# Kernel tuning notes

Hardware: AMD Instinct MI355X
Metric: run time of the kernel (lower is better)

The kernel has to match this reference:

```python
import jax, jax.numpy as jnp
import numpy as np

N, E, H = 50000, 300000, 8  # nodes, edges, FeaStConv heads (PyG default)


def _lin_init(k, fan_in, fan_out):
    k1, k2 = jax.random.split(k)
    s = 1.0 / np.sqrt(fan_in)
    w = jax.random.uniform(k1, (fan_in, fan_out), jnp.float32, -s, s)
    b = jax.random.uniform(k2, (fan_out,), jnp.float32, -s, s)
    return w, b


def _conv_init(k, cin, cout):
    k1, k2 = jax.random.split(k)
    w = jax.random.normal(k1, (cin, H * cout), jnp.float32) * 0.1   # weight
    u = jax.random.normal(k2, (cin, H), jnp.float32) * 0.1          # attention u
    c = jnp.zeros((H,), jnp.float32)                                 # attention bias
    b = jnp.zeros((cout,), jnp.float32)                              # output bias
    return w, u, c, b


def setup_inputs() -> dict:
    key = jax.random.key(0)
    ks = jax.random.split(key, 10)
    x = jax.random.normal(ks[0], (N, 3), jnp.float32)
    src = jax.random.randint(ks[1], (E,), 0, N)
    dst = jax.random.randint(ks[2], (E,), 0, N)
    dst = jnp.where(src == dst, (dst + 1) % N, dst)  # no self loops in raw edge list
    edge_index = jnp.stack([src, dst]).astype(jnp.int64)
    labels = (jax.random.uniform(ks[3], (N, 1)) < 0.1).astype(jnp.float32)
    lin1_w, lin1_b = _lin_init(ks[4], 3, 16)
    c1_w, c1_u, c1_c, c1_b = _conv_init(ks[5], 16, 32)
    c2_w, c2_u, c2_c, c2_b = _conv_init(ks[6], 32, 64)
    c3_w, c3_u, c3_c, c3_b = _conv_init(ks[7], 64, 128)
    lin2_w, lin2_b = _lin_init(ks[8], 128, 1024)
    lin3_w, lin3_b = _lin_init(ks[9], 1024, 1)
    return dict(x=x, edge_index=edge_index, labels=labels,
                lin1_w=lin1_w, lin1_b=lin1_b,
                c1_w=c1_w, c1_u=c1_u, c1_c=c1_c, c1_b=c1_b,
                c2_w=c2_w, c2_u=c2_u, c2_c=c2_c, c2_b=c2_b,
                c3_w=c3_w, c3_u=c3_u, c3_c=c3_c, c3_b=c3_b,
                lin2_w=lin2_w, lin2_b=lin2_b, lin3_w=lin3_w, lin3_b=lin3_b)


def feast_conv(x, src, dst, W, u, c, b):
    """PyG FeaStConv: gather x_i/x_j, head-softmax attention on (x_j - x_i),
    per-edge weighted sum over heads, mean-scatter to destination nodes."""
    n = x.shape[0]
    loop = jnp.arange(n, dtype=src.dtype)
    s = jnp.concatenate([src, loop])  # add self loops (PyG default)
    d = jnp.concatenate([dst, loop])
    xi = x[d]
    xj = x[s]
    q = jax.nn.softmax((xj - xi) @ u + c, axis=-1)           # [E+N, H]
    m = (xj @ W).reshape(xj.shape[0], H, -1)                  # [E+N, H, O]
    msg = jnp.einsum('eh,eho->eo', q, m)                      # [E+N, O]
    agg = jax.ops.segment_sum(msg, d, num_segments=n)
    cnt = jax.ops.segment_sum(jnp.ones_like(d, dtype=msg.dtype), d, num_segments=n)
    return agg / cnt[:, None] + b                             # mean aggregation + bias


def reference(x, edge_index, labels,
              lin1_w, lin1_b,
              c1_w, c1_u, c1_c, c1_b,
              c2_w, c2_u, c2_c, c2_b,
              c3_w, c3_u, c3_c, c3_b,
              lin2_w, lin2_b, lin3_w, lin3_b):
    src, dst = edge_index[0], edge_index[1]
    h = jax.nn.relu(x @ lin1_w + lin1_b)
    h = jax.nn.relu(feast_conv(h, src, dst, c1_w, c1_u, c1_c, c1_b))
    h = jax.nn.relu(feast_conv(h, src, dst, c2_w, c2_u, c2_c, c2_b))
    h = jax.nn.relu(feast_conv(h, src, dst, c3_w, c3_u, c3_c, c3_b))
    h = jax.nn.relu(h @ lin2_w + lin2_b)
    p = jax.nn.sigmoid(h @ lin3_w + lin3_b)                   # [N, 1]
    # generate_weights: class-balanced per-element BCE weights
    n = labels.shape[0]
    pos = jnp.sum(labels)
    neg = n - pos
    w = jnp.where(labels == 1, n / (2.0 * pos), n / (2.0 * neg))
    # torch-style BCE with log clamped at -100
    bce = -(labels * jnp.clip(jnp.log(p), -100.0, None)
            + (1.0 - labels) * jnp.clip(jnp.log(1.0 - p), -100.0, None))
    loss = jnp.mean(w * bce)
    return loss, p
```

## Files before the change

kernel.cpp:

```cpp
#include <hip/hip_runtime.h>
#include <math.h>

#define NN 50000
#define NE 300000

typedef short s8v __attribute__((ext_vector_type(8)));
typedef float f4v __attribute__((ext_vector_type(4)));

__device__ inline unsigned short f2bf(float f) {
    union { float f; unsigned int u; } v; v.f = f;
    unsigned int r = v.u + 0x7FFFu + ((v.u >> 16) & 1u);
    return (unsigned short)(r >> 16);
}
__device__ inline float bf2f(unsigned short u) {
    union { unsigned int i; float f; } v; v.i = ((unsigned int)u) << 16;
    return v.f;
}

template<int CIN, int O>
__device__ inline void packw_feast_body(const float* __restrict__ W,
                                        unsigned short* __restrict__ wp, int t) {
    constexpr int NS = (8*CIN) / 32;
    int l = t & 63;
    int s = (t >> 6) % NS;
    int ct = t / (64 * NS);
    int c = ct*16 + (l & 15);
    int kk0 = s*32 + (l >> 4) * 8;
    union { unsigned short u[8]; s8v v; } o;
    #pragma unroll
    for (int i = 0; i < 8; ++i) {
        int kk = kk0 + i;
        int h = kk / CIN, k = kk & (CIN - 1);
        o.u[i] = f2bf(W[(size_t)k*(8*O) + h*O + c]);
    }
    *(s8v*)(wp + (size_t)t*8) = o.v;
}

__device__ inline void packw_lin_body(const float* __restrict__ W,
                                      unsigned short* __restrict__ wp, int t) {
    int l = t & 63;
    int s = (t >> 6) & 3;
    int ctg = t >> 8;
    int c = ctg*16 + (l & 15);
    int k0 = s*32 + (l >> 4) * 8;
    union { unsigned short u[8]; s8v v; } o;
    #pragma unroll
    for (int i = 0; i < 8; ++i) o.u[i] = f2bf(W[(size_t)(k0+i)*1024 + c]);
    *(s8v*)(wp + (size_t)t*8) = o.v;
}

__global__ __launch_bounds__(256) void prep_kernel(
        const float* __restrict__ l2w, unsigned short* __restrict__ w2p,
        const float* __restrict__ wf1w, unsigned short* __restrict__ wf1,
        const float* __restrict__ wf2w, unsigned short* __restrict__ wf2,
        const float* __restrict__ wf3w, unsigned short* __restrict__ wf3,
        int* __restrict__ fill, int* __restrict__ fill2,
        float* __restrict__ z, float* __restrict__ scal,
        const float* __restrict__ x, const float* __restrict__ l1w,
        const float* __restrict__ l1b, const float* __restrict__ u1,
        unsigned short* __restrict__ h1, float* __restrict__ a) {
    __shared__ float hsh[16][16];
    int b = blockIdx.x;
    int tid = threadIdx.x;
    if (b < 64)  { packw_lin_body(l2w, w2p, b*256 + tid); return; }
    b -= 64;
    if (b < 2)   { packw_feast_body<16,32>(wf1w, wf1, b*256 + tid); return; }
    b -= 2;
    if (b < 8)   { packw_feast_body<32,64>(wf2w, wf2, b*256 + tid); return; }
    b -= 8;
    if (b < 32)  { packw_feast_body<64,128>(wf3w, wf3, b*256 + tid); return; }
    b -= 32;
    if (b < 587) {
        int idx = b*256 + tid;
        if (idx < NN)            fill[idx] = 0;
        else if (idx < 2*NN)     fill2[idx - NN] = 0;
        else if (idx < 3*NN)     z[idx - 2*NN] = 0.f;
        else if (idx < 3*NN+16)  scal[idx - 3*NN] = 0.f;
        return;
    }
    b -= 587;
    int n0 = b * 16;
    int node = n0 + (tid >> 4), col = tid & 15;
    float v = x[node*3+0]*l1w[col] + x[node*3+1]*l1w[16+col]
            + x[node*3+2]*l1w[32+col] + l1b[col];
    v = fmaxf(v, 0.f);
    h1[(size_t)node*16 + col] = f2bf(v);
    hsh[tid >> 4][col] = v;
    __syncthreads();
    if (tid < 128) {
        int t2 = tid >> 3, h = tid & 7;
        float acc = 0.f;
        #pragma unroll
        for (int k = 0; k < 16; ++k) acc += hsh[t2][k] * u1[k*8 + h];
        a[(size_t)(n0 + t2)*8 + h] = acc;
    }
}

__global__ void hist_kernel(const int* __restrict__ dst, int* __restrict__ cnt) {
    int e = blockIdx.x * 256 + threadIdx.x;
    if (e < NE) atomicAdd(&cnt[dst[e]], 1);
}

__global__ void scan1_kernel(const int* __restrict__ cnt, int* __restrict__ rp,
                             int* __restrict__ bpart) {
    __shared__ int sh[256];
    int tid = threadIdx.x;
    int gid = blockIdx.x * 256 + tid;
    int v = (gid < NN) ? cnt[gid] : 0;
    sh[tid] = v;
    __syncthreads();
    for (int off = 1; off < 256; off <<= 1) {
        int t = (tid >= off) ? sh[tid - off] : 0;
        __syncthreads();
        sh[tid] += t;
        __syncthreads();
    }
    if (gid < NN) rp[gid] = sh[tid] - v;
    if (tid == 255) bpart[blockIdx.x] = sh[tid];
}

__global__ void scanfix_kernel(int* __restrict__ rp, const int* __restrict__ bpart,
                               int nblk) {
    __shared__ int sh[256];
    int tid = threadIdx.x;
    int bx = blockIdx.x;
    sh[tid] = (tid < bx && tid < nblk) ? bpart[tid] : 0;
    __syncthreads();
    for (int off = 128; off; off >>= 1) {
        if (tid < off) sh[tid] += sh[tid + off];
        __syncthreads();
    }
    int add = sh[0];
    int gid = bx * 256 + tid;
    if (gid < NN) rp[gid] += add;
    if (gid == 0) rp[NN] = NE;
}

__global__ void scatter_kernel(const int* __restrict__ src, const int* __restrict__ dst,
                               const int* __restrict__ rp, int* __restrict__ fill,
                               int* __restrict__ ssrc) {
    int e = blockIdx.x * 256 + threadIdx.x;
    if (e >= NE) return;
    int d = dst[e];
    int pos = rp[d] + atomicAdd(&fill[d], 1);
    ssrc[pos] = src[e];
}

template<int CIN>
__global__ __launch_bounds__(256) void agg_kernel(
        const unsigned short* __restrict__ hin, const float* __restrict__ a,
        const float* __restrict__ cbias,
        const int* __restrict__ rowptr, const int* __restrict__ ssrc,
        unsigned short* __restrict__ g) {
    constexpr int HPER = CIN / 8;
    constexpr int LG = (CIN == 16) ? 4 : (CIN == 32) ? 5 : 6;
    __shared__ float qsh[4][64][8];
    const int lane = threadIdx.x & 63;
    const int w = threadIdx.x >> 6;
    const int d = blockIdx.x * 4 + w;
    const int k = lane & (CIN - 1);
    const int hg = lane >> LG;
    float cc[8], ad[8];
    #pragma unroll
    for (int h = 0; h < 8; ++h) { cc[h] = cbias[h]; ad[h] = a[(size_t)d*8 + h]; }
    float m0 = cc[0];
    #pragma unroll
    for (int h = 1; h < 8; ++h) m0 = fmaxf(m0, cc[h]);
    float ssum = 0.f;
    #pragma unroll
    for (int h = 0; h < 8; ++h) ssum += __expf(cc[h] - m0);
    float sinv = 1.f / ssum;
    float xd = bf2f(hin[(size_t)d*CIN + k]);
    float acc[HPER];
    #pragma unroll
    for (int i = 0; i < HPER; ++i)
        acc[i] = __expf(cc[hg*HPER + i] - m0) * sinv * xd;
    const int j0 = rowptr[d], j1 = rowptr[d+1];
    for (int jb = j0; jb < j1; jb += 64) {
        int cnt = j1 - jb; if (cnt > 64) cnt = 64;
        if (lane < cnt) {
            int s = ssrc[jb + lane];
            const float4* as = (const float4*)(a + (size_t)s*8);
            float4 s0 = as[0], s1 = as[1];
            float lg[8] = { s0.x-ad[0]+cc[0], s0.y-ad[1]+cc[1],
                            s0.z-ad[2]+cc[2], s0.w-ad[3]+cc[3],
                            s1.x-ad[4]+cc[4], s1.y-ad[5]+cc[5],
                            s1.z-ad[6]+cc[6], s1.w-ad[7]+cc[7] };
            float m = lg[0];
            #pragma unroll
            for (int h = 1; h < 8; ++h) m = fmaxf(m, lg[h]);
            float sum = 0.f;
            #pragma unroll
            for (int h = 0; h < 8; ++h) { lg[h] = __expf(lg[h]-m); sum += lg[h]; }
            float inv = 1.f / sum;
            float4* qp = (float4*)&qsh[w][lane][0];
            qp[0] = make_float4(lg[0]*inv, lg[1]*inv, lg[2]*inv, lg[3]*inv);
            qp[1] = make_float4(lg[4]*inv, lg[5]*inv, lg[6]*inv, lg[7]*inv);
        }
        int je = jb + cnt;
        int j = jb;
        for (; j + 2 <= je; j += 2) {
            int s0 = ssrc[j], s1 = ssrc[j+1];
            float xv0 = bf2f(hin[(size_t)s0*CIN + k]);
            float xv1 = bf2f(hin[(size_t)s1*CIN + k]);
            float qv0[HPER], qv1[HPER];
            if constexpr (HPER == 2) {
                float2 t0 = *(const float2*)&qsh[w][j-jb][hg*2];
                float2 t1 = *(const float2*)&qsh[w][j+1-jb][hg*2];
                qv0[0]=t0.x; qv0[1]=t0.y; qv1[0]=t1.x; qv1[1]=t1.y;
            } else if constexpr (HPER == 4) {
                float4 t0 = *(const float4*)&qsh[w][j-jb][hg*4];
                float4 t1 = *(const float4*)&qsh[w][j+1-jb][hg*4];
                qv0[0]=t0.x; qv0[1]=t0.y; qv0[2]=t0.z; qv0[3]=t0.w;
                qv1[0]=t1.x; qv1[1]=t1.y; qv1[2]=t1.z; qv1[3]=t1.w;
            } else {
                float4 t0a = *(const float4*)&qsh[w][j-jb][0];
                float4 t0b = *(const float4*)&qsh[w][j-jb][4];
                float4 t1a = *(const float4*)&qsh[w][j+1-jb][0];
                float4 t1b = *(const float4*)&qsh[w][j+1-jb][4];
                qv0[0]=t0a.x; qv0[1]=t0a.y; qv0[2]=t0a.z; qv0[3]=t0a.w;
                qv0[4]=t0b.x; qv0[5]=t0b.y; qv0[6]=t0b.z; qv0[7]=t0b.w;
                qv1[0]=t1a.x; qv1[1]=t1a.y; qv1[2]=t1a.z; qv1[3]=t1a.w;
                qv1[4]=t1b.x; qv1[5]=t1b.y; qv1[6]=t1b.z; qv1[7]=t1b.w;
            }
            #pragma unroll
            for (int i = 0; i < HPER; ++i) acc[i] += qv0[i]*xv0 + qv1[i]*xv1;
        }
        if (j < je) {
            int s0 = ssrc[j];
            float xv0 = bf2f(hin[(size_t)s0*CIN + k]);
            #pragma unroll
            for (int i = 0; i < HPER; ++i)
                acc[i] += qsh[w][j-jb][hg*HPER + i] * xv0;
        }
    }
    #pragma unroll
    for (int i = 0; i < HPER; ++i)
        g[(size_t)d*(8*CIN) + (hg*HPER + i)*CIN + k] = f2bf(acc[i]);
}

template<int K, int O, int CH, bool AEPI>
__global__ __launch_bounds__(256) void gemm_feast(
        const unsigned short* __restrict__ g, const unsigned short* __restrict__ wp,
        const int* __restrict__ rowptr, const float* __restrict__ b,
        unsigned short* __restrict__ hout,
        const float* __restrict__ unext, float* __restrict__ aout) {
    constexpr int NS = K / 32;
    constexpr int NCT = O / 16;
    __shared__ unsigned short bsh[CH*NS*64*8];
    const int l = threadIdx.x & 63;
    const int w = threadIdx.x >> 6;
    const int base = blockIdx.x * 64 + w * 16;
    int arow = base + (l & 15); if (arow >= NN) arow = NN - 1;
    const int koff = (l >> 4) * 8;
    s8v af[NS];
    #pragma unroll
    for (int s = 0; s < NS; ++s)
        af[s] = *(const s8v*)(g + (size_t)arow*K + s*32 + koff);
    float invc[4];
    #pragma unroll
    for (int r = 0; r < 4; ++r) {
        int n = base + (l >> 4)*4 + r; if (n >= NN) n = NN - 1;
        invc[r] = 1.f / (float)(rowptr[n+1] - rowptr[n] + 1);
    }
    float apart[4][8];
    if constexpr (AEPI) {
        #pragma unroll
        for (int r = 0; r < 4; ++r)
            #pragma unroll
            for (int h = 0; h < 8; ++h) apart[r][h] = 0.f;
    }
    #pragma unroll 1
    for (int ct0 = 0; ct0 < NCT; ct0 += CH) {
        __syncthreads();
        const int4* sp = (const int4*)(wp + (size_t)ct0*NS*512);
        int4* dp = (int4*)bsh;
        #pragma unroll 1
        for (int i = threadIdx.x; i < CH*NS*64; i += 256) dp[i] = sp[i];
        __syncthreads();
        #pragma unroll 1
        for (int cc = 0; cc < CH; ++cc) {
            f4v accA = {0.f,0.f,0.f,0.f}, accB = {0.f,0.f,0.f,0.f};
            #pragma unroll
            for (int s = 0; s < NS/2; ++s) {
                s8v bf = *(const s8v*)(bsh + ((size_t)(cc*NS + s)*64 + l)*8);
                accA = __builtin_amdgcn_mfma_f32_16x16x32_bf16(af[s], bf, accA, 0, 0, 0);
            }
            #pragma unroll
            for (int s = NS/2; s < NS; ++s) {
                s8v bf = *(const s8v*)(bsh + ((size_t)(cc*NS + s)*64 + l)*8);
                accB = __builtin_amdgcn_mfma_f32_16x16x32_bf16(af[s], bf, accB, 0, 0, 0);
            }
            int col = (ct0 + cc)*16 + (l & 15);
            float bb = b[col];
            float uv[8];
            if constexpr (AEPI) {
                #pragma unroll
                for (int h = 0; h < 8; ++h) uv[h] = unext[col*8 + h];
            }
            #pragma unroll
            for (int r = 0; r < 4; ++r) {
                int n = base + (l >> 4)*4 + r;
                float v = fmaxf((accA[r]+accB[r])*invc[r] + bb, 0.f);
                if constexpr (AEPI) {
                    #pragma unroll
                    for (int h = 0; h < 8; ++h) apart[r][h] += v * uv[h];
                }
                if (n < NN) hout[(size_t)n*O + col] = f2bf(v);
            }
        }
    }
    if constexpr (AEPI) {
        #pragma unroll
        for (int r = 0; r < 4; ++r)
            #pragma unroll
            for (int h = 0; h < 8; ++h) {
                float v = apart[r][h];
                v += __shfl_xor(v, 1, 64);
                v += __shfl_xor(v, 2, 64);
                v += __shfl_xor(v, 4, 64);
                v += __shfl_xor(v, 8, 64);
                if ((l & 15) == 0) {
                    int n = base + (l >> 4)*4 + r;
                    if (n < NN) aout[(size_t)n*8 + h] = v;
                }
            }
    }
}

__global__ __launch_bounds__(256) void lin23z_kernel(
        const unsigned short* __restrict__ h4b, const unsigned short* __restrict__ w2p,
        const float* __restrict__ b2, const float* __restrict__ w3,
        float* __restrict__ z) {
    const int l = threadIdx.x & 63;
    const int w = threadIdx.x >> 6;
    const int ctg = blockIdx.y;
    const int rowbase = blockIdx.x * 256 + w * 64;
    const int koff = (l >> 4) * 8;
    s8v bf0[4], bf1[4], bf2[4], bf3[4];
    #pragma unroll
    for (int s = 0; s < 4; ++s) {
        bf0[s] = *(const s8v*)(w2p + ((size_t)((ctg*4+0)*4 + s)*64 + l)*8);
        bf1[s] = *(const s8v*)(w2p + ((size_t)((ctg*4+1)*4 + s)*64 + l)*8);
        bf2[s] = *(const s8v*)(w2p + ((size_t)((ctg*4+2)*4 + s)*64 + l)*8);
        bf3[s] = *(const s8v*)(w2p + ((size_t)((ctg*4+3)*4 + s)*64 + l)*8);
    }
    float w3c[4], b2c[4];
    #pragma unroll
    for (int c = 0; c < 4; ++c) {
        int col = (ctg*4 + c)*16 + (l & 15);
        w3c[c] = w3[col]; b2c[c] = b2[col];
    }
    #pragma unroll 1
    for (int t = 0; t < 4; ++t) {
        int base = rowbase + t*16;
        int arow = base + (l & 15); if (arow >= NN) arow = NN - 1;
        s8v af[4];
        #pragma unroll
        for (int s = 0; s < 4; ++s)
            af[s] = *(const s8v*)(h4b + (size_t)arow*128 + s*32 + koff);
        float zp0 = 0.f, zp1 = 0.f, zp2 = 0.f, zp3 = 0.f;
        #pragma unroll
        for (int c = 0; c < 4; ++c) {
            const s8v* bf = (c == 0) ? bf0 : (c == 1) ? bf1 : (c == 2) ? bf2 : bf3;
            f4v accA = {0.f,0.f,0.f,0.f}, accB = {0.f,0.f,0.f,0.f};
            accA = __builtin_amdgcn_mfma_f32_16x16x32_bf16(af[0], bf[0], accA, 0, 0, 0);
            accA = __builtin_amdgcn_mfma_f32_16x16x32_bf16(af[1], bf[1], accA, 0, 0, 0);
            accB = __builtin_amdgcn_mfma_f32_16x16x32_bf16(af[2], bf[2], accB, 0, 0, 0);
            accB = __builtin_amdgcn_mfma_f32_16x16x32_bf16(af[3], bf[3], accB, 0, 0, 0);
            zp0 += fmaxf(accA[0]+accB[0] + b2c[c], 0.f) * w3c[c];
            zp1 += fmaxf(accA[1]+accB[1] + b2c[c], 0.f) * w3c[c];
            zp2 += fmaxf(accA[2]+accB[2] + b2c[c], 0.f) * w3c[c];
            zp3 += fmaxf(accA[3]+accB[3] + b2c[c], 0.f) * w3c[c];
        }
        #pragma unroll
        for (int m = 1; m < 16; m <<= 1) {
            zp0 += __shfl_xor(zp0, m, 64);
            zp1 += __shfl_xor(zp1, m, 64);
            zp2 += __shfl_xor(zp2, m, 64);
            zp3 += __shfl_xor(zp3, m, 64);
        }
        if ((l & 15) == 0) {
            int r0 = base + (l >> 4) * 4;
            if (r0+0 < NN) atomicAdd(&z[r0+0], zp0);
            if (r0+1 < NN) atomicAdd(&z[r0+1], zp1);
            if (r0+2 < NN) atomicAdd(&z[r0+2], zp2);
            if (r0+3 < NN) atomicAdd(&z[r0+3], zp3);
        }
    }
}

__global__ void finish_kernel(const float* __restrict__ labels,
                              const float* __restrict__ z,
                              const float* __restrict__ b3,
                              float* __restrict__ p,
                              float* __restrict__ scal,
                              float* __restrict__ out, int nblk) {
    __shared__ float sh0[256], sh1[256], sh2[256];
    int tid = threadIdx.x;
    int n = blockIdx.x * 256 + tid;
    float pos = 0.f, sp = 0.f, sn = 0.f;
    if (n < NN) {
        float pv = 1.f / (1.f + expf(-(z[n] + b3[0])));
        p[n] = pv;
        float yv = labels[n];
        if (yv == 1.0f) { pos = 1.f; sp = -fmaxf(logf(pv), -100.f); }
        else            { sn = -fmaxf(logf(1.f - pv), -100.f); }
    }
    sh0[tid] = pos; sh1[tid] = sp; sh2[tid] = sn;
    __syncthreads();
    for (int off = 128; off; off >>= 1) {
        if (tid < off) {
            sh0[tid] += sh0[tid+off];
            sh1[tid] += sh1[tid+off];
            sh2[tid] += sh2[tid+off];
        }
        __syncthreads();
    }
    if (tid == 0) {
        atomicAdd(&scal[0], sh0[0]);
        atomicAdd(&scal[1], sh1[0]);
        atomicAdd(&scal[2], sh2[0]);
        __threadfence();
        int t = atomicAdd((int*)&scal[4], 1);
        if (t == nblk - 1) {
            float posT = atomicAdd(&scal[0], 0.f);
            float spT  = atomicAdd(&scal[1], 0.f);
            float snT  = atomicAdd(&scal[2], 0.f);
            out[0] = spT / (2.f*posT) + snT / (2.f*((float)NN - posT));
        }
    }
}

extern "C" void kernel_launch(void* const* d_in, const int* in_sizes, int n_in,
                              void* d_out, int out_size, void* d_ws, size_t ws_size,
                              hipStream_t stream) {
    (void)in_sizes; (void)n_in; (void)out_size; (void)ws_size;
    const float* x   = (const float*)d_in[0];
    const int*   ei  = (const int*)d_in[1];
    const float* labels = (const float*)d_in[2];
    const float* l1w = (const float*)d_in[3];
    const float* l1b = (const float*)d_in[4];
    const float* cw[3] = {(const float*)d_in[5], (const float*)d_in[9],  (const float*)d_in[13]};
    const float* cu[3] = {(const float*)d_in[6], (const float*)d_in[10], (const float*)d_in[14]};
    const float* cc[3] = {(const float*)d_in[7], (const float*)d_in[11], (const float*)d_in[15]};
    const float* cb[3] = {(const float*)d_in[8], (const float*)d_in[12], (const float*)d_in[16]};
    const float* l2w = (const float*)d_in[17];
    const float* l2b = (const float*)d_in[18];
    const float* l3w = (const float*)d_in[19];
    const float* l3b = (const float*)d_in[20];
    const int* srcp = ei;
    const int* dstp = ei + NE;
    float* out = (float*)d_out;

    float* ws = (float*)d_ws;
    size_t off = 0;
    auto alloc = [&](size_t n) { float* p = ws + off; off += (n + 15) & ~(size_t)15; return p; };
    unsigned short* hA = (unsigned short*)alloc((size_t)NN*32);
    unsigned short* hB = (unsigned short*)alloc((size_t)NN*64);
    float* a  = alloc((size_t)NN*8);
    unsigned short* g   = (unsigned short*)alloc((size_t)NN*256);
    unsigned short* w2p = (unsigned short*)alloc(65536);
    unsigned short* wf1 = (unsigned short*)alloc(2048);
    unsigned short* wf2 = (unsigned short*)alloc(8192);
    unsigned short* wf3 = (unsigned short*)alloc(32768);
    float* z    = alloc(NN);
    float* scal = alloc(16);
    int* rowptr = (int*)alloc(50016);
    int* fill   = (int*)alloc(NN);
    int* fill2  = (int*)alloc(NN);
    int* ssrc   = (int*)alloc(NE);
    int* bpart  = (int*)alloc(256);

    const int SCAN_BLKS = (NN + 255) / 256;
    const int GB = (NN + 63) / 64;
    const int PREP_BLKS = 106 + 587 + NN/16;

    prep_kernel<<<PREP_BLKS, 256, 0, stream>>>(l2w, w2p, cw[0], wf1, cw[1], wf2,
                                               cw[2], wf3, fill, fill2, z, scal,
                                               x, l1w, l1b, cu[0], hA, a);
    hist_kernel<<<(NE+255)/256, 256, 0, stream>>>(dstp, fill);
    scan1_kernel<<<SCAN_BLKS, 256, 0, stream>>>(fill, rowptr, bpart);
    scanfix_kernel<<<SCAN_BLKS, 256, 0, stream>>>(rowptr, bpart, SCAN_BLKS);
    scatter_kernel<<<(NE+255)/256, 256, 0, stream>>>(srcp, dstp, rowptr, fill2, ssrc);

    agg_kernel<16><<<NN/4, 256, 0, stream>>>(hA, a, cc[0], rowptr, ssrc, g);
    gemm_feast<128,32,2,true><<<GB, 256, 0, stream>>>(g, wf1, rowptr, cb[0], hB, cu[1], a);

    agg_kernel<32><<<NN/4, 256, 0, stream>>>(hB, a, cc[1], rowptr, ssrc, g);
    gemm_feast<256,64,4,true><<<GB, 256, 0, stream>>>(g, wf2, rowptr, cb[1], hA, cu[2], a);

    agg_kernel<64><<<NN/4, 256, 0, stream>>>(hA, a, cc[2], rowptr, ssrc, g);
    gemm_feast<512,128,2,false><<<GB, 256, 0, stream>>>(g, wf3, rowptr, cb[2], hB, nullptr, nullptr);

    lin23z_kernel<<<dim3((NN+255)/256, 16), 256, 0, stream>>>(hB, w2p, l2b, l3w, z);
    finish_kernel<<<SCAN_BLKS, 256, 0, stream>>>(labels, z, l3b, out + 1, scal, out, SCAN_BLKS);
}
```

Before: 246.3 us.

## Fuse FeaStConv aggregation and MFMA GEMM into a single per-layer kernel

Merges agg_kernel and gemm_feast into one conv_kernel per layer. Each block aggregates 64 destination rows into an XOR-swizzled LDS tile and then runs the bf16 MFMA GEMM straight from LDS, so the large intermediate g buffer is never written to or read back from global memory. The attention buffer is now double-buffered (aA/aB) because the fused kernel reads the current layer's attention logits while writing the next layer's. The trade-off is that each wave now aggregates 16 rows serially, and the larger LDS footprint lowers occupancy, which can expose gather latency. Layer 2's weight chunk count also drops from 4 to 1.

```diff
diff --git a/kernel.cpp b/kernel.cpp
--- a/kernel.cpp
+++ b/kernel.cpp
@@ -146,23 +146,29 @@
     ssrc[pos] = src[e];
 }
 
-template<int CIN>
-__global__ __launch_bounds__(256) void agg_kernel(
+template<int CIN, int O, int CH, bool AEPI>
+__global__ __launch_bounds__(256) void conv_kernel(
         const unsigned short* __restrict__ hin, const float* __restrict__ a,
         const float* __restrict__ cbias,
         const int* __restrict__ rowptr, const int* __restrict__ ssrc,
-        unsigned short* __restrict__ g) {
+        const unsigned short* __restrict__ wp, const float* __restrict__ b,
+        unsigned short* __restrict__ hout,
+        const float* __restrict__ unext, float* __restrict__ aout) {
+    constexpr int K = 8*CIN;
+    constexpr int NS = K / 32;
+    constexpr int NCT = O / 16;
     constexpr int HPER = CIN / 8;
     constexpr int LG = (CIN == 16) ? 4 : (CIN == 32) ? 5 : 6;
-    __shared__ float qsh[4][64][8];
-    const int lane = threadIdx.x & 63;
+    __shared__ unsigned short gt[64 * K];
+    __shared__ unsigned short bsh[CH * NS * 512];
+    const int l = threadIdx.x & 63;
     const int w = threadIdx.x >> 6;
-    const int d = blockIdx.x * 4 + w;
-    const int k = lane & (CIN - 1);
-    const int hg = lane >> LG;
-    float cc[8], ad[8];
-    #pragma unroll
-    for (int h = 0; h < 8; ++h) { cc[h] = cbias[h]; ad[h] = a[(size_t)d*8 + h]; }
+    float* qsh = (float*)bsh + w*512;
+    const int k = l & (CIN - 1);
+    const int hg = l >> LG;
+    float cc[8];
+    #pragma unroll
+    for (int h = 0; h < 8; ++h) cc[h] = cbias[h];
     float m0 = cc[0];
     #pragma unroll
     for (int h = 1; h < 8; ++h) m0 = fmaxf(m0, cc[h]);
@@ -170,93 +176,101 @@
     #pragma unroll
     for (int h = 0; h < 8; ++h) ssum += __expf(cc[h] - m0);
     float sinv = 1.f / ssum;
-    float xd = bf2f(hin[(size_t)d*CIN + k]);
-    float acc[HPER];
-    #pragma unroll
-    for (int i = 0; i < HPER; ++i)
-        acc[i] = __expf(cc[hg*HPER + i] - m0) * sinv * xd;
-    const int j0 = rowptr[d], j1 = rowptr[d+1];
-    for (int jb = j0; jb < j1; jb += 64) {
-        int cnt = j1 - jb; if (cnt > 64) cnt = 64;
-        if (lane < cnt) {
-            int s = ssrc[jb + lane];
-            const float4* as = (const float4*)(a + (size_t)s*8);
-            float4 s0 = as[0], s1 = as[1];
-            float lg[8] = { s0.x-ad[0]+cc[0], s0.y-ad[1]+cc[1],
-                            s0.z-ad[2]+cc[2], s0.w-ad[3]+cc[3],
-                            s1.x-ad[4]+cc[4], s1.y-ad[5]+cc[5],
-                            s1.z-ad[6]+cc[6], s1.w-ad[7]+cc[7] };
-            float m = lg[0];
-            #pragma unroll
-            for (int h = 1; h < 8; ++h) m = fmaxf(m, lg[h]);
-            float sum = 0.f;
-            #pragma unroll
-            for (int h = 0; h < 8; ++h) { lg[h] = __expf(lg[h]-m); sum += lg[h]; }
-            float inv = 1.f / sum;
-            float4* qp = (float4*)&qsh[w][lane][0];
-            qp[0] = make_float4(lg[0]*inv, lg[1]*inv, lg[2]*inv, lg[3]*inv);
-            qp[1] = make_float4(lg[4]*inv, lg[5]*inv, lg[6]*inv, lg[7]*inv);
-        }
-        int je = jb + cnt;
-        int j = jb;
-        for (; j + 2 <= je; j += 2) {
-            int s0 = ssrc[j], s1 = ssrc[j+1];
-            float xv0 = bf2f(hin[(size_t)s0*CIN + k]);
-            float xv1 = bf2f(hin[(size_t)s1*CIN + k]);
-            float qv0[HPER], qv1[HPER];
-            if constexpr (HPER == 2) {
-                float2 t0 = *(const float2*)&qsh[w][j-jb][hg*2];
-                float2 t1 = *(const float2*)&qsh[w][j+1-jb][hg*2];
-                qv0[0]=t0.x; qv0[1]=t0.y; qv1[0]=t1.x; qv1[1]=t1.y;
-            } else if constexpr (HPER == 4) {
-                float4 t0 = *(const float4*)&qsh[w][j-jb][hg*4];
-                float4 t1 = *(const float4*)&qsh[w][j+1-jb][hg*4];
-                qv0[0]=t0.x; qv0[1]=t0.y; qv0[2]=t0.z; qv0[3]=t0.w;
-                qv1[0]=t1.x; qv1[1]=t1.y; qv1[2]=t1.z; qv1[3]=t1.w;
-            } else {
-                float4 t0a = *(const float4*)&qsh[w][j-jb][0];
-                float4 t0b = *(const float4*)&qsh[w][j-jb][4];
-                float4 t1a = *(const float4*)&qsh[w][j+1-jb][0];
-                float4 t1b = *(const float4*)&qsh[w][j+1-jb][4];
-                qv0[0]=t0a.x; qv0[1]=t0a.y; qv0[2]=t0a.z; qv0[3]=t0a.w;
-                qv0[4]=t0b.x; qv0[5]=t0b.y; qv0[6]=t0b.z; qv0[7]=t0b.w;
-                qv1[0]=t1a.x; qv1[1]=t1a.y; qv1[2]=t1a.z; qv1[3]=t1a.w;
-                qv1[4]=t1b.x; qv1[5]=t1b.y; qv1[6]=t1b.z; qv1[7]=t1b.w;
-            }
-            #pragma unroll
-            for (int i = 0; i < HPER; ++i) acc[i] += qv0[i]*xv0 + qv1[i]*xv1;
-        }
-        if (j < je) {
-            int s0 = ssrc[j];
-            float xv0 = bf2f(hin[(size_t)s0*CIN + k]);
+    float scv[HPER];
+    #pragma unroll
+    for (int i = 0; i < HPER; ++i) scv[i] = __expf(cc[hg*HPER + i] - m0) * sinv;
+
+    for (int r16 = 0; r16 < 16; ++r16) {
+        const int row = w*16 + r16;
+        unsigned short* grow = gt + row * K;
+        const int swz = (row & 7) << 3;
+        const int d = blockIdx.x * 64 + row;
+        if (d >= NN) {
             #pragma unroll
             for (int i = 0; i < HPER; ++i)
-                acc[i] += qsh[w][j-jb][hg*HPER + i] * xv0;
-        }
-    }
-    #pragma unroll
-    for (int i = 0; i < HPER; ++i)
-        g[(size_t)d*(8*CIN) + (hg*HPER + i)*CIN + k] = f2bf(acc[i]);
-}
-
-template<int K, int O, int CH, bool AEPI>
-__global__ __launch_bounds__(256) void gemm_feast(
-        const unsigned short* __restrict__ g, const unsigned short* __restrict__ wp,
-        const int* __restrict__ rowptr, const float* __restrict__ b,
-        unsigned short* __restrict__ hout,
-        const float* __restrict__ unext, float* __restrict__ aout) {
-    constexpr int NS = K / 32;
-    constexpr int NCT = O / 16;
-    __shared__ unsigned short bsh[CH*NS*64*8];
-    const int l = threadIdx.x & 63;
-    const int w = threadIdx.x >> 6;
+                grow[((hg*HPER + i)*CIN + k) ^ swz] = 0;
+            continue;
+        }
+        float ad[8];
+        #pragma unroll
+        for (int h = 0; h < 8; ++h) ad[h] = a[(size_t)d*8 + h];
+        float xd = bf2f(hin[(size_t)d*CIN + k]);
+        float acc[HPER];
+        #pragma unroll
+        for (int i = 0; i < HPER; ++i) acc[i] = scv[i] * xd;
+        const int j0 = rowptr[d], j1 = rowptr[d+1];
+        for (int jb = j0; jb < j1; jb += 64) {
+            int cnt = j1 - jb; if (cnt > 64) cnt = 64;
+            if (l < cnt) {
+                int s = ssrc[jb + l];
+                const float4* as = (const float4*)(a + (size_t)s*8);
+                float4 s0 = as[0], s1 = as[1];
+                float lg[8] = { s0.x-ad[0]+cc[0], s0.y-ad[1]+cc[1],
+                                s0.z-ad[2]+cc[2], s0.w-ad[3]+cc[3],
+                                s1.x-ad[4]+cc[4], s1.y-ad[5]+cc[5],
+                                s1.z-ad[6]+cc[6], s1.w-ad[7]+cc[7] };
+                float m = lg[0];
+                #pragma unroll
+                for (int h = 1; h < 8; ++h) m = fmaxf(m, lg[h]);
+                float sum = 0.f;
+                #pragma unroll
+                for (int h = 0; h < 8; ++h) { lg[h] = __expf(lg[h]-m); sum += lg[h]; }
+                float inv = 1.f / sum;
+                float4* qp = (float4*)&qsh[l*8];
+                qp[0] = make_float4(lg[0]*inv, lg[1]*inv, lg[2]*inv, lg[3]*inv);
+                qp[1] = make_float4(lg[4]*inv, lg[5]*inv, lg[6]*inv, lg[7]*inv);
+            }
+            int je = jb + cnt;
+            int j = jb;
+            for (; j + 2 <= je; j += 2) {
+                int s0 = ssrc[j], s1 = ssrc[j+1];
+                float xv0 = bf2f(hin[(size_t)s0*CIN + k]);
+                float xv1 = bf2f(hin[(size_t)s1*CIN + k]);
+                float qv0[HPER], qv1[HPER];
+                if constexpr (HPER == 2) {
+                    float2 t0 = *(const float2*)&qsh[(j-jb)*8 + hg*2];
+                    float2 t1 = *(const float2*)&qsh[(j+1-jb)*8 + hg*2];
+                    qv0[0]=t0.x; qv0[1]=t0.y; qv1[0]=t1.x; qv1[1]=t1.y;
+                } else if constexpr (HPER == 4) {
+                    float4 t0 = *(const float4*)&qsh[(j-jb)*8 + hg*4];
+                    float4 t1 = *(const float4*)&qsh[(j+1-jb)*8 + hg*4];
+                    qv0[0]=t0.x; qv0[1]=t0.y; qv0[2]=t0.z; qv0[3]=t0.w;
+                    qv1[0]=t1.x; qv1[1]=t1.y; qv1[2]=t1.z; qv1[3]=t1.w;
+                } else {
+                    float4 t0a = *(const float4*)&qsh[(j-jb)*8];
+                    float4 t0b = *(const float4*)&qsh[(j-jb)*8 + 4];
+                    float4 t1a = *(const float4*)&qsh[(j+1-jb)*8];
+                    float4 t1b = *(const float4*)&qsh[(j+1-jb)*8 + 4];
+                    qv0[0]=t0a.x; qv0[1]=t0a.y; qv0[2]=t0a.z; qv0[3]=t0a.w;
+                    qv0[4]=t0b.x; qv0[5]=t0b.y; qv0[6]=t0b.z; qv0[7]=t0b.w;
+                    qv1[0]=t1a.x; qv1[1]=t1a.y; qv1[2]=t1a.z; qv1[3]=t1a.w;
+                    qv1[4]=t1b.x; qv1[5]=t1b.y; qv1[6]=t1b.z; qv1[7]=t1b.w;
+                }
+                #pragma unroll
+                for (int i = 0; i < HPER; ++i) acc[i] += qv0[i]*xv0 + qv1[i]*xv1;
+            }
+            if (j < je) {
+                int s0 = ssrc[j];
+                float xv0 = bf2f(hin[(size_t)s0*CIN + k]);
+                #pragma unroll
+                for (int i = 0; i < HPER; ++i)
+                    acc[i] += qsh[(j-jb)*8 + hg*HPER + i] * xv0;
+            }
+        }
+        #pragma unroll
+        for (int i = 0; i < HPER; ++i)
+            grow[((hg*HPER + i)*CIN + k) ^ swz] = f2bf(acc[i]);
+    }
+
     const int base = blockIdx.x * 64 + w * 16;
-    int arow = base + (l & 15); if (arow >= NN) arow = NN - 1;
-    const int koff = (l >> 4) * 8;
     s8v af[NS];
-    #pragma unroll
-    for (int s = 0; s < NS; ++s)
-        af[s] = *(const s8v*)(g + (size_t)arow*K + s*32 + koff);
+    {
+        const int row = w*16 + (l & 15);
+        const int swz = (row & 7) << 3;
+        #pragma unroll
+        for (int s = 0; s < NS; ++s)
+            af[s] = *(const s8v*)(gt + row*K + ((s*32 + (l >> 4)*8) ^ swz));
+    }
     float invc[4];
     #pragma unroll
     for (int r = 0; r < 4; ++r) {
@@ -279,19 +293,19 @@
         for (int i = threadIdx.x; i < CH*NS*64; i += 256) dp[i] = sp[i];
         __syncthreads();
         #pragma unroll 1
-        for (int cc = 0; cc < CH; ++cc) {
+        for (int cc_ = 0; cc_ < CH; ++cc_) {
             f4v accA = {0.f,0.f,0.f,0.f}, accB = {0.f,0.f,0.f,0.f};
             #pragma unroll
             for (int s = 0; s < NS/2; ++s) {
-                s8v bf = *(const s8v*)(bsh + ((size_t)(cc*NS + s)*64 + l)*8);
+                s8v bf = *(const s8v*)(bsh + ((size_t)(cc_*NS + s)*64 + l)*8);
                 accA = __builtin_amdgcn_mfma_f32_16x16x32_bf16(af[s], bf, accA, 0, 0, 0);
             }
             #pragma unroll
             for (int s = NS/2; s < NS; ++s) {
-                s8v bf = *(const s8v*)(bsh + ((size_t)(cc*NS + s)*64 + l)*8);
+                s8v bf = *(const s8v*)(bsh + ((size_t)(cc_*NS + s)*64 + l)*8);
                 accB = __builtin_amdgcn_mfma_f32_16x16x32_bf16(af[s], bf, accB, 0, 0, 0);
             }
-            int col = (ct0 + cc)*16 + (l & 15);
+            int col = (ct0 + cc_)*16 + (l & 15);
             float bb = b[col];
             float uv[8];
             if constexpr (AEPI) {
@@ -458,8 +472,8 @@
     auto alloc = [&](size_t n) { float* p = ws + off; off += (n + 15) & ~(size_t)15; return p; };
     unsigned short* hA = (unsigned short*)alloc((size_t)NN*32);
     unsigned short* hB = (unsigned short*)alloc((size_t)NN*64);
-    float* a  = alloc((size_t)NN*8);
-    unsigned short* g   = (unsigned short*)alloc((size_t)NN*256);
+    float* aA = alloc((size_t)NN*8);
+    float* aB = alloc((size_t)NN*8);
     unsigned short* w2p = (unsigned short*)alloc(65536);
     unsigned short* wf1 = (unsigned short*)alloc(2048);
     unsigned short* wf2 = (unsigned short*)alloc(8192);
@@ -478,20 +492,18 @@
 
     prep_kernel<<<PREP_BLKS, 256, 0, stream>>>(l2w, w2p, cw[0], wf1, cw[1], wf2,
                                                cw[2], wf3, fill, fill2, z, scal,
-                                               x, l1w, l1b, cu[0], hA, a);
+                                               x, l1w, l1b, cu[0], hA, aA);
     hist_kernel<<<(NE+255)/256, 256, 0, stream>>>(dstp, fill);
     scan1_kernel<<<SCAN_BLKS, 256, 0, stream>>>(fill, rowptr, bpart);
     scanfix_kernel<<<SCAN_BLKS, 256, 0, stream>>>(rowptr, bpart, SCAN_BLKS);
     scatter_kernel<<<(NE+255)/256, 256, 0, stream>>>(srcp, dstp, rowptr, fill2, ssrc);
 
-    agg_kernel<16><<<NN/4, 256, 0, stream>>>(hA, a, cc[0], rowptr, ssrc, g);
-    gemm_feast<128,32,2,true><<<GB, 256, 0, stream>>>(g, wf1, rowptr, cb[0], hB, cu[1], a);
-
-    agg_kernel<32><<<NN/4, 256, 0, stream>>>(hB, a, cc[1], rowptr, ssrc, g);
-    gemm_feast<256,64,4,true><<<GB, 256, 0, stream>>>(g, wf2, rowptr, cb[1], hA, cu[2], a);
-
-    agg_kernel<64><<<NN/4, 256, 0, stream>>>(hA, a, cc[2], rowptr, ssrc, g);
-    gemm_feast<512,128,2,false><<<GB, 256, 0, stream>>>(g, wf3, rowptr, cb[2], hB, nullptr, nullptr);
+    conv_kernel<16,32,2,true ><<<GB, 256, 0, stream>>>(hA, aA, cc[0], rowptr, ssrc,
+                                                       wf1, cb[0], hB, cu[1], aB);
+    conv_kernel<32,64,1,true ><<<GB, 256, 0, stream>>>(hB, aB, cc[1], rowptr, ssrc,
+                                                       wf2, cb[1], hA, cu[2], aA);
+    conv_kernel<64,128,1,false><<<GB, 256, 0, stream>>>(hA, aA, cc[2], rowptr, ssrc,
+                                                        wf3, cb[2], hB, nullptr, nullptr);
 
     lin23z_kernel<<<dim3((NN+255)/256, 16), 256, 0, stream>>>(hB, w2p, l2b, l3w, z);
     finish_kernel<<<SCAN_BLKS, 256, 0, stream>>>(labels, z, l3b, out + 1, scal, out, SCAN_BLKS);
```

Result: slower. 351.6 us (+42.8%).
